# Performance work log

Measured on AMD Instinct MI355X. Metric: run time of the kernel, lower is better.

The kernel has to match this reference:

```python
import jax, jax.numpy as jnp
import numpy as np

N_NODES = 50000
N_EDGES = 800000
N_GRAPHS = 64
IN_C = 64
HID = 64
NEG_SLOPE = 0.2  # PyG GATConv default


def setup_inputs() -> dict:
    key = jax.random.key(0)
    ks = jax.random.split(key, 12)
    x = jax.random.normal(ks[0], (N_NODES, IN_C), dtype=jnp.float32)
    edge_index = jax.random.randint(ks[1], (2, N_EDGES), 0, N_NODES, dtype=jnp.int64)
    batch = jnp.sort(jax.random.randint(ks[2], (N_NODES,), 0, N_GRAPHS, dtype=jnp.int64))
    s = 1.0 / np.sqrt(IN_C)
    sh = 1.0 / np.sqrt(HID)
    W = jax.random.uniform(ks[3], (IN_C, HID), jnp.float32, -s, s)
    att_src = jax.random.uniform(ks[4], (HID,), jnp.float32, -sh, sh)
    att_dst = jax.random.uniform(ks[5], (HID,), jnp.float32, -sh, sh)
    bias_gat = jnp.zeros((HID,), jnp.float32)
    w1 = jax.random.uniform(ks[6], (HID, HID), jnp.float32, -sh, sh)
    b1 = jax.random.uniform(ks[7], (HID,), jnp.float32, -sh, sh)
    w2 = jax.random.uniform(ks[8], (HID, 1), jnp.float32, -sh, sh)
    b2 = jax.random.uniform(ks[9], (1,), jnp.float32, -sh, sh)
    return {"x": x, "edge_index": edge_index, "batch": batch, "W": W,
            "att_src": att_src, "att_dst": att_dst, "bias_gat": bias_gat,
            "w1": w1, "b1": b1, "w2": w2, "b2": b2}


def _gat_conv(x, edge_index, W, att_src, att_dst, bias_gat):
    N = x.shape[0]
    # add self-loops (PyG default)
    loops = jnp.arange(N, dtype=edge_index.dtype)
    src = jnp.concatenate([edge_index[0], loops])  # message source j
    dst = jnp.concatenate([edge_index[1], loops])  # message target i
    h = x @ W                                      # [N, HID]
    a_s = h @ att_src                              # [N]
    a_d = h @ att_dst                              # [N]
    e = jax.nn.leaky_relu(a_s[src] + a_d[dst], negative_slope=NEG_SLOPE)  # [E+N]
    # segment softmax over incoming edges of each target node
    m = jax.ops.segment_max(e, dst, num_segments=N)
    ex = jnp.exp(e - m[dst])
    denom = jax.ops.segment_sum(ex, dst, num_segments=N)
    alpha = ex / denom[dst]
    out = jax.ops.segment_sum(h[src] * alpha[:, None], dst, num_segments=N)
    return out + bias_gat


def reference(x, edge_index, batch, W, att_src, att_dst, bias_gat, w1, b1, w2, b2):
    h = jax.nn.relu(_gat_conv(x, edge_index, W, att_src, att_dst, bias_gat))
    # global mean pool over each graph
    sums = jax.ops.segment_sum(h, batch, num_segments=N_GRAPHS)          # [G, HID]
    cnt = jax.ops.segment_sum(jnp.ones((h.shape[0],), h.dtype), batch,
                              num_segments=N_GRAPHS)
    pooled = sums / jnp.maximum(cnt, 1.0)[:, None]
    z = jax.nn.relu(pooled @ w1 + b1)
    z = z @ w2 + b2
    return jax.nn.sigmoid(z)  # [G, 1]
```

## Files before the change

kernel.cpp:

```cpp
#include <hip/hip_runtime.h>

#define NN 50000
#define NE 800000
#define NG 64
#define HID 64
#define NEG 0.2f
#define NPW 64
#define NBUCK 196
#define CHUNK 2048
#define KC_CAP 6144

__global__ __launch_bounds__(256)
void k_xw(const float* __restrict__ x, const float* __restrict__ W,
          const float* __restrict__ att_s, const float* __restrict__ att_d,
          float* __restrict__ h, float* __restrict__ as_, float* __restrict__ ad_,
          int* __restrict__ gcur) {
    __shared__ __align__(16) float sW[64][64];
    __shared__ __align__(16) float sxT[64][68];
    int t = threadIdx.x;
    if (blockIdx.x == 0 && t < NBUCK) gcur[t] = 0;
    int r0 = blockIdx.x * 64;
    for (int i = t; i < 4096; i += 256) sW[i >> 6][i & 63] = W[i];
    for (int i = t; i < 4096; i += 256) {
        int r = i >> 6, c = i & 63;
        int gr = r0 + r; if (gr >= NN) gr = NN - 1;
        sxT[c][r] = x[(size_t)gr * 64 + c];
    }
    __syncthreads();

    int tx = t & 15, ty = t >> 4;
    float4 asv = ((const float4*)att_s)[tx];
    float4 adv = ((const float4*)att_d)[tx];

    float acc[4][4] = {};
    #pragma unroll
    for (int k = 0; k < 64; ++k) {
        float4 a = *(const float4*)&sxT[k][4 * ty];
        float4 b = *(const float4*)&sW[k][4 * tx];
        float av[4] = {a.x, a.y, a.z, a.w};
        float bv[4] = {b.x, b.y, b.z, b.w};
        #pragma unroll
        for (int i = 0; i < 4; ++i)
            #pragma unroll
            for (int j = 0; j < 4; ++j)
                acc[i][j] += av[i] * bv[j];
    }

    #pragma unroll
    for (int i = 0; i < 4; ++i) {
        int r = r0 + 4 * ty + i;
        if (r < NN) {
            float4 hv = make_float4(acc[i][0], acc[i][1], acc[i][2], acc[i][3]);
            *(float4*)&h[(size_t)r * 64 + 4 * tx] = hv;
            float ps = acc[i][0]*asv.x + acc[i][1]*asv.y + acc[i][2]*asv.z + acc[i][3]*asv.w;
            float pd = acc[i][0]*adv.x + acc[i][1]*adv.y + acc[i][2]*adv.z + acc[i][3]*adv.w;
            #pragma unroll
            for (int m = 1; m <= 8; m <<= 1) {
                ps += __shfl_xor(ps, m, 64);
                pd += __shfl_xor(pd, m, 64);
            }
            if (tx == 0) { as_[r] = ps; ad_[r] = pd; }
        }
    }
}

__global__ __launch_bounds__(256)
void k_bucket(const int* __restrict__ src, const int* __restrict__ dst,
              int* __restrict__ gcur, int* __restrict__ ebuf) {
    __shared__ int lhist[256], lscan[256], loff[256], lcur[256], gbase[256];
    __shared__ int lsort[CHUNK];
    __shared__ unsigned char lbuck[CHUNK];
    int t = threadIdx.x;
    int base = blockIdx.x * CHUNK;
    int cnt = NE - base; if (cnt > CHUNK) cnt = CHUNK; if (cnt < 0) cnt = 0;

    int ds[8], ss[8];
    int nv = 0;
    #pragma unroll
    for (int j = 0; j < 8; ++j) {
        int e = base + j * 256 + t;
        if (e < NE) { ds[nv] = dst[e]; ss[nv] = src[e]; ++nv; }
    }
    lhist[t] = 0;
    __syncthreads();
    for (int j = 0; j < nv; ++j) atomicAdd(&lhist[ds[j] >> 8], 1);
    __syncthreads();
    lscan[t] = lhist[t];
    __syncthreads();
    for (int off = 1; off < 256; off <<= 1) {
        int u = (t >= off) ? lscan[t - off] : 0;
        __syncthreads();
        lscan[t] += u;
        __syncthreads();
    }
    loff[t] = lscan[t] - lhist[t];
    lcur[t] = 0;
    __syncthreads();
    for (int j = 0; j < nv; ++j) {
        int b = ds[j] >> 8;
        int r = atomicAdd(&lcur[b], 1);
        int slot = loff[b] + r;
        lsort[slot] = (ss[j] << 8) | (ds[j] & 255);
        lbuck[slot] = (unsigned char)b;
    }
    if (t < NBUCK) {
        int c = lhist[t];
        gbase[t] = c ? atomicAdd(&gcur[t], c) : 0;
    }
    __syncthreads();
    for (int i = t; i < cnt; i += 256) {
        int b = lbuck[i];
        ebuf[b * KC_CAP + gbase[b] + (i - loff[b])] = lsort[i];
    }
}

__global__ __launch_bounds__(256)
void k_csr(const int* __restrict__ gcur, const int* __restrict__ ebuf,
           int* __restrict__ csr, int* __restrict__ cursor, int* __restrict__ deg) {
    __shared__ int lhist[256], lscan[256], loff[256], lcur[256], bscan[256];
    __shared__ int lsrc[KC_CAP];
    int t = threadIdx.x;
    int b = blockIdx.x;

    bscan[t] = (t < NBUCK) ? gcur[t] : 0;
    __syncthreads();
    for (int off = 1; off < 256; off <<= 1) {
        int u = (t >= off) ? bscan[t - off] : 0;
        __syncthreads();
        bscan[t] += u;
        __syncthreads();
    }
    int sz = gcur[b];
    int gb = bscan[b] - sz;
    const int* seg = ebuf + b * KC_CAP;

    lhist[t] = 0;
    __syncthreads();
    for (int i = t; i < sz; i += 256)
        atomicAdd(&lhist[seg[i] & 255], 1);
    __syncthreads();
    lscan[t] = lhist[t];
    __syncthreads();
    for (int off = 1; off < 256; off <<= 1) {
        int u = (t >= off) ? lscan[t - off] : 0;
        __syncthreads();
        lscan[t] += u;
        __syncthreads();
    }
    loff[t] = lscan[t] - lhist[t];
    lcur[t] = 0;
    __syncthreads();
    for (int i = t; i < sz; i += 256) {
        int w = seg[i];
        int dl = w & 255;
        int r = atomicAdd(&lcur[dl], 1);
        lsrc[loff[dl] + r] = w >> 8;
    }
    __syncthreads();
    for (int i = t; i < sz; i += 256)
        csr[gb + i] = lsrc[i];
    int d = b * 256 + t;
    if (d < NN) {
        deg[d] = lhist[t];
        cursor[d] = gb + loff[t] + lhist[t];
    }
}

__global__ __launch_bounds__(256)
void k_gather(const int* __restrict__ csr, const int* __restrict__ cursor,
              const int* __restrict__ deg, const float* __restrict__ h,
              const float* __restrict__ as_, const float* __restrict__ ad_,
              const float* __restrict__ bias, float* __restrict__ g,
              float* __restrict__ poolz) {
    int t = threadIdx.x;
    if (blockIdx.x == 0) {
        for (int i = t; i < NG * HID + NG; i += 256) poolz[i] = 0.f;
    }
    int wave = t >> 6, lane = t & 63;
    int d = blockIdx.x * 4 + wave;
    if (d >= NN) return;
    int cend = cursor[d];
    int nd   = deg[d];
    int cbeg = cend - nd;
    float adv = ad_[d];
    float e0 = as_[d] + adv;
    e0 = e0 >= 0.f ? e0 : NEG * e0;
    float ex0 = __expf(e0);
    float den = ex0;
    float acc = h[(size_t)d * 64 + lane] * ex0;
    #pragma unroll 4
    for (int c = cbeg; c < cend; ++c) {
        int s = csr[c];
        float av = as_[s] + adv;
        av = av >= 0.f ? av : NEG * av;
        float ex = __expf(av);
        den += ex;
        acc += h[(size_t)s * 64 + lane] * ex;
    }
    g[(size_t)d * 64 + lane] = fmaxf(acc / den + bias[lane], 0.f);
}

__global__ __launch_bounds__(256)
void k_node(const float* __restrict__ g, const int* __restrict__ batch,
            float* __restrict__ pooled, float* __restrict__ cnt) {
    int t = threadIdx.x;
    int wave = t >> 6, lane = t & 63;
    int n0 = (blockIdx.x * 4 + wave) * NPW;
    if (n0 >= NN) return;
    int n1 = n0 + NPW; if (n1 > NN) n1 = NN;
    float acc = 0.f, c = 0.f;
    int cur = batch[n0];
    for (int n = n0; n < n1; ++n) {
        int gr = batch[n];
        if (gr != cur) {
            atomicAdd(&pooled[cur * 64 + lane], acc);
            if (lane == 0) atomicAdd(&cnt[cur], c);
            acc = 0.f; c = 0.f; cur = gr;
        }
        acc += g[(size_t)n * 64 + lane];
        c += 1.f;
    }
    atomicAdd(&pooled[cur * 64 + lane], acc);
    if (lane == 0) atomicAdd(&cnt[cur], c);
}

__global__ __launch_bounds__(256)
void k_final(const float* __restrict__ pooled, const float* __restrict__ cnt,
             const float* __restrict__ w1, const float* __restrict__ b1,
             const float* __restrict__ w2, const float* __restrict__ b2,
             float* __restrict__ out) {
    __shared__ float sp[64][65];
    __shared__ float sz[64][65];
    int t = threadIdx.x;
    for (int i = t; i < 4096; i += 256) {
        int g = i >> 6, c = i & 63;
        sp[g][c] = pooled[i] / fmaxf(cnt[g], 1.0f);
    }
    __syncthreads();
    for (int i = t; i < 4096; i += 256) {
        int g = i >> 6, c = i & 63;
        float acc = b1[c];
        #pragma unroll
        for (int k = 0; k < 64; ++k) acc += sp[g][k] * w1[k * 64 + c];
        sz[g][c] = fmaxf(acc, 0.f);
    }
    __syncthreads();
    if (t < 64) {
        float acc = b2[0];
        #pragma unroll
        for (int c = 0; c < 64; ++c) acc += sz[t][c] * w2[c];
        out[t] = 1.f / (1.f + __expf(-acc));
    }
}

extern "C" void kernel_launch(void* const* d_in, const int* in_sizes, int n_in,
                              void* d_out, int out_size, void* d_ws, size_t ws_size,
                              hipStream_t stream) {
    const float* x     = (const float*)d_in[0];
    const int*   ei    = (const int*)d_in[1];
    const int*   batch = (const int*)d_in[2];
    const float* W     = (const float*)d_in[3];
    const float* att_s = (const float*)d_in[4];
    const float* att_d = (const float*)d_in[5];
    const float* bias  = (const float*)d_in[6];
    const float* w1    = (const float*)d_in[7];
    const float* b1    = (const float*)d_in[8];
    const float* w2    = (const float*)d_in[9];
    const float* b2    = (const float*)d_in[10];
    float* out = (float*)d_out;

    const int* src = ei;
    const int* dst = ei + NE;

    float* h      = (float*)d_ws;
    float* as_    = h + (size_t)NN * HID;
    float* ad_    = as_ + NN;
    float* g      = ad_ + NN;
    float* pooled = g + (size_t)NN * HID;
    float* cntp   = pooled + NG * HID;
    int*   deg    = (int*)(cntp + NG);
    int*   cursor = deg + NN;
    int*   csr    = cursor + NN;
    int*   gcur   = csr + NE;
    int*   ebuf   = (int*)g;


    k_xw<<<(NN + 63) / 64, 256, 0, stream>>>(x, W, att_s, att_d, h, as_, ad_, gcur);

    k_bucket<<<(NE + CHUNK - 1) / CHUNK, 256, 0, stream>>>(src, dst, gcur, ebuf);
    k_csr<<<NBUCK, 256, 0, stream>>>(gcur, ebuf, csr, cursor, deg);

    k_gather<<<(NN + 3) / 4, 256, 0, stream>>>(csr, cursor, deg, h, as_, ad_, bias, g, pooled);

    k_node<<<(NN / (4 * NPW)) + 1, 256, 0, stream>>>(g, batch, pooled, cntp);

    k_final<<<1, 256, 0, stream>>>(pooled, cntp, w1, b1, w2, b2, out);
}
```

Before: 143.8 us.

## Fuse CSR build, gather and pooling into one bucketed LDS-accumulate kernel with bf16 features

Drops the separate CSR sort, per-node gather and pooling kernels. Each block now owns a 128-node bucket and accumulates exp-weighted messages into shared memory with LDS atomics, then applies the normalization, ReLU and pooling directly. The edge exp weights are computed during bucketing and stored alongside the packed src/dst, and h is stored as bf16 to halve gather bandwidth. This removes the intermediate CSR and g buffers and several launches. The cost is only 392 blocks of parallelism, heavy LDS atomic contention, and reduced precision of h, which may affect tolerance.

```diff
diff --git a/kernel.cpp b/kernel.cpp
--- a/kernel.cpp
+++ b/kernel.cpp
@@ -1,24 +1,37 @@
 #include <hip/hip_runtime.h>
+#include <hip/hip_bf16.h>
 
 #define NN 50000
 #define NE 800000
 #define NG 64
 #define HID 64
 #define NEG 0.2f
-#define NPW 64
-#define NBUCK 196
+#define NBUCK 392
 #define CHUNK 2048
-#define KC_CAP 6144
+#define KC_CAP 3072
+#define ROWP 66
+
+__device__ __forceinline__ unsigned short f2bf(float f) {
+    unsigned int u = __float_as_uint(f);
+    unsigned int r = (u + 0x7FFF + ((u >> 16) & 1)) >> 16;
+    return (unsigned short)r;
+}
+__device__ __forceinline__ float bf_lo(unsigned int p) { return __uint_as_float(p << 16); }
+__device__ __forceinline__ float bf_hi(unsigned int p) { return __uint_as_float(p & 0xFFFF0000u); }
+__device__ __forceinline__ float bf2f(unsigned short b) { return __uint_as_float(((unsigned int)b) << 16); }
 
 __global__ __launch_bounds__(256)
 void k_xw(const float* __restrict__ x, const float* __restrict__ W,
           const float* __restrict__ att_s, const float* __restrict__ att_d,
-          float* __restrict__ h, float* __restrict__ as_, float* __restrict__ ad_,
-          int* __restrict__ gcur) {
+          unsigned short* __restrict__ hb, float* __restrict__ as_, float* __restrict__ ad_,
+          int* __restrict__ gcur, float* __restrict__ poolz) {
     __shared__ __align__(16) float sW[64][64];
     __shared__ __align__(16) float sxT[64][68];
     int t = threadIdx.x;
-    if (blockIdx.x == 0 && t < NBUCK) gcur[t] = 0;
+    if (blockIdx.x == 0) {
+        for (int i = t; i < NBUCK; i += 256) gcur[i] = 0;
+        for (int i = t; i < NG * HID + NG; i += 256) poolz[i] = 0.f;
+    }
     int r0 = blockIdx.x * 64;
     for (int i = t; i < 4096; i += 256) sW[i >> 6][i & 63] = W[i];
     for (int i = t; i < 4096; i += 256) {
@@ -50,8 +63,10 @@
     for (int i = 0; i < 4; ++i) {
         int r = r0 + 4 * ty + i;
         if (r < NN) {
-            float4 hv = make_float4(acc[i][0], acc[i][1], acc[i][2], acc[i][3]);
-            *(float4*)&h[(size_t)r * 64 + 4 * tx] = hv;
+            ushort4 hv;
+            hv.x = f2bf(acc[i][0]); hv.y = f2bf(acc[i][1]);
+            hv.z = f2bf(acc[i][2]); hv.w = f2bf(acc[i][3]);
+            *(ushort4*)&hb[(size_t)r * 64 + 4 * tx] = hv;
             float ps = acc[i][0]*asv.x + acc[i][1]*asv.y + acc[i][2]*asv.z + acc[i][3]*asv.w;
             float pd = acc[i][0]*adv.x + acc[i][1]*adv.y + acc[i][2]*adv.z + acc[i][3]*adv.w;
             #pragma unroll
@@ -64,30 +79,37 @@
     }
 }
 
-__global__ __launch_bounds__(256)
+__global__ __launch_bounds__(512)
 void k_bucket(const int* __restrict__ src, const int* __restrict__ dst,
-              int* __restrict__ gcur, int* __restrict__ ebuf) {
-    __shared__ int lhist[256], lscan[256], loff[256], lcur[256], gbase[256];
-    __shared__ int lsort[CHUNK];
-    __shared__ unsigned char lbuck[CHUNK];
+              const float* __restrict__ as_, const float* __restrict__ ad_,
+              int* __restrict__ gcur, int2* __restrict__ ebuf) {
+    __shared__ int lhist[512], lscan[512], loff[512], lcur[512], gbase[512];
+    __shared__ int2 lsort[CHUNK];
+    __shared__ unsigned short lbuck[CHUNK];
     int t = threadIdx.x;
     int base = blockIdx.x * CHUNK;
     int cnt = NE - base; if (cnt > CHUNK) cnt = CHUNK; if (cnt < 0) cnt = 0;
 
-    int ds[8], ss[8];
+    int ds[4], ss[4];
+    float ex[4];
     int nv = 0;
     #pragma unroll
-    for (int j = 0; j < 8; ++j) {
-        int e = base + j * 256 + t;
+    for (int j = 0; j < 4; ++j) {
+        int e = base + j * 512 + t;
         if (e < NE) { ds[nv] = dst[e]; ss[nv] = src[e]; ++nv; }
     }
+    for (int j = 0; j < nv; ++j) {
+        float e = as_[ss[j]] + ad_[ds[j]];
+        e = e >= 0.f ? e : NEG * e;
+        ex[j] = __expf(e);
+    }
     lhist[t] = 0;
     __syncthreads();
-    for (int j = 0; j < nv; ++j) atomicAdd(&lhist[ds[j] >> 8], 1);
+    for (int j = 0; j < nv; ++j) atomicAdd(&lhist[ds[j] >> 7], 1);
     __syncthreads();
     lscan[t] = lhist[t];
     __syncthreads();
-    for (int off = 1; off < 256; off <<= 1) {
+    for (int off = 1; off < 512; off <<= 1) {
         int u = (t >= off) ? lscan[t - off] : 0;
         __syncthreads();
         lscan[t] += u;
@@ -97,131 +119,94 @@
     lcur[t] = 0;
     __syncthreads();
     for (int j = 0; j < nv; ++j) {
-        int b = ds[j] >> 8;
+        int b = ds[j] >> 7;
         int r = atomicAdd(&lcur[b], 1);
         int slot = loff[b] + r;
-        lsort[slot] = (ss[j] << 8) | (ds[j] & 255);
-        lbuck[slot] = (unsigned char)b;
+        lsort[slot] = make_int2((ss[j] << 7) | (ds[j] & 127), __float_as_int(ex[j]));
+        lbuck[slot] = (unsigned short)b;
     }
     if (t < NBUCK) {
         int c = lhist[t];
         gbase[t] = c ? atomicAdd(&gcur[t], c) : 0;
     }
     __syncthreads();
-    for (int i = t; i < cnt; i += 256) {
+    for (int i = t; i < cnt; i += 512) {
         int b = lbuck[i];
         ebuf[b * KC_CAP + gbase[b] + (i - loff[b])] = lsort[i];
     }
 }
 
 __global__ __launch_bounds__(256)
-void k_csr(const int* __restrict__ gcur, const int* __restrict__ ebuf,
-           int* __restrict__ csr, int* __restrict__ cursor, int* __restrict__ deg) {
-    __shared__ int lhist[256], lscan[256], loff[256], lcur[256], bscan[256];
-    __shared__ int lsrc[KC_CAP];
-    int t = threadIdx.x;
+void k_merged(const int* __restrict__ gcur, const int2* __restrict__ ebuf,
+              const unsigned short* __restrict__ hb,
+              const float* __restrict__ as_, const float* __restrict__ ad_,
+              const float* __restrict__ bias, const int* __restrict__ batch,
+              float* __restrict__ pooled, float* __restrict__ cnt) {
+    __shared__ float lacc[128 * ROWP];
+    __shared__ float lden[128];
+    int t = threadIdx.x;
+    int wave = t >> 6, lane = t & 63;
+    int grp = lane >> 3, cc = lane & 7;
     int b = blockIdx.x;
 
-    bscan[t] = (t < NBUCK) ? gcur[t] : 0;
-    __syncthreads();
-    for (int off = 1; off < 256; off <<= 1) {
-        int u = (t >= off) ? bscan[t - off] : 0;
-        __syncthreads();
-        bscan[t] += u;
-        __syncthreads();
-    }
+    for (int i = t; i < 128 * ROWP; i += 256) lacc[i] = 0.f;
+    if (t < 128) lden[t] = 0.f;
+    __syncthreads();
+
     int sz = gcur[b];
-    int gb = bscan[b] - sz;
-    const int* seg = ebuf + b * KC_CAP;
-
-    lhist[t] = 0;
-    __syncthreads();
-    for (int i = t; i < sz; i += 256)
-        atomicAdd(&lhist[seg[i] & 255], 1);
-    __syncthreads();
-    lscan[t] = lhist[t];
-    __syncthreads();
-    for (int off = 1; off < 256; off <<= 1) {
-        int u = (t >= off) ? lscan[t - off] : 0;
-        __syncthreads();
-        lscan[t] += u;
-        __syncthreads();
-    }
-    loff[t] = lscan[t] - lhist[t];
-    lcur[t] = 0;
-    __syncthreads();
-    for (int i = t; i < sz; i += 256) {
-        int w = seg[i];
-        int dl = w & 255;
-        int r = atomicAdd(&lcur[dl], 1);
-        lsrc[loff[dl] + r] = w >> 8;
-    }
-    __syncthreads();
-    for (int i = t; i < sz; i += 256)
-        csr[gb + i] = lsrc[i];
-    int d = b * 256 + t;
-    if (d < NN) {
-        deg[d] = lhist[t];
-        cursor[d] = gb + loff[t] + lhist[t];
-    }
-}
-
-__global__ __launch_bounds__(256)
-void k_gather(const int* __restrict__ csr, const int* __restrict__ cursor,
-              const int* __restrict__ deg, const float* __restrict__ h,
-              const float* __restrict__ as_, const float* __restrict__ ad_,
-              const float* __restrict__ bias, float* __restrict__ g,
-              float* __restrict__ poolz) {
-    int t = threadIdx.x;
-    if (blockIdx.x == 0) {
-        for (int i = t; i < NG * HID + NG; i += 256) poolz[i] = 0.f;
-    }
-    int wave = t >> 6, lane = t & 63;
-    int d = blockIdx.x * 4 + wave;
-    if (d >= NN) return;
-    int cend = cursor[d];
-    int nd   = deg[d];
-    int cbeg = cend - nd;
-    float adv = ad_[d];
-    float e0 = as_[d] + adv;
-    e0 = e0 >= 0.f ? e0 : NEG * e0;
-    float ex0 = __expf(e0);
-    float den = ex0;
-    float acc = h[(size_t)d * 64 + lane] * ex0;
-    #pragma unroll 4
-    for (int c = cbeg; c < cend; ++c) {
-        int s = csr[c];
-        float av = as_[s] + adv;
-        av = av >= 0.f ? av : NEG * av;
-        float ex = __expf(av);
-        den += ex;
-        acc += h[(size_t)s * 64 + lane] * ex;
-    }
-    g[(size_t)d * 64 + lane] = fmaxf(acc / den + bias[lane], 0.f);
-}
-
-__global__ __launch_bounds__(256)
-void k_node(const float* __restrict__ g, const int* __restrict__ batch,
-            float* __restrict__ pooled, float* __restrict__ cnt) {
-    int t = threadIdx.x;
-    int wave = t >> 6, lane = t & 63;
-    int n0 = (blockIdx.x * 4 + wave) * NPW;
-    if (n0 >= NN) return;
-    int n1 = n0 + NPW; if (n1 > NN) n1 = NN;
-    float acc = 0.f, c = 0.f;
-    int cur = batch[n0];
-    for (int n = n0; n < n1; ++n) {
-        int gr = batch[n];
+    const int2* seg = ebuf + b * KC_CAP;
+
+    for (int i0 = wave * 8; i0 < sz; i0 += 32) {
+        int e = i0 + grp;
+        if (e < sz) {
+            int2 w = seg[e];
+            int   s  = w.x >> 7;
+            int   dl = w.x & 127;
+            float ex = __int_as_float(w.y);
+            uint4 v = *(const uint4*)&hb[(size_t)s * 64 + 8 * cc];
+            float* a = &lacc[dl * ROWP + 8 * cc];
+            atomicAdd(a + 0, bf_lo(v.x) * ex);
+            atomicAdd(a + 1, bf_hi(v.x) * ex);
+            atomicAdd(a + 2, bf_lo(v.y) * ex);
+            atomicAdd(a + 3, bf_hi(v.y) * ex);
+            atomicAdd(a + 4, bf_lo(v.z) * ex);
+            atomicAdd(a + 5, bf_hi(v.z) * ex);
+            atomicAdd(a + 6, bf_lo(v.w) * ex);
+            atomicAdd(a + 7, bf_hi(v.w) * ex);
+            if (cc == 0) atomicAdd(&lden[dl], ex);
+        }
+    }
+    __syncthreads();
+
+    float bl = bias[lane];
+    int dbase = b * 128 + wave * 32;
+    float racc = 0.f, rcnt = 0.f;
+    int cur = -1;
+    for (int k = 0; k < 32; ++k) {
+        int d = dbase + k;
+        if (d >= NN) break;
+        int gr = batch[d];
         if (gr != cur) {
-            atomicAdd(&pooled[cur * 64 + lane], acc);
-            if (lane == 0) atomicAdd(&cnt[cur], c);
-            acc = 0.f; c = 0.f; cur = gr;
+            if (cur >= 0) {
+                atomicAdd(&pooled[cur * 64 + lane], racc);
+                if (lane == 0) atomicAdd(&cnt[cur], rcnt);
+            }
+            racc = 0.f; rcnt = 0.f; cur = gr;
         }
-        acc += g[(size_t)n * 64 + lane];
-        c += 1.f;
-    }
-    atomicAdd(&pooled[cur * 64 + lane], acc);
-    if (lane == 0) atomicAdd(&cnt[cur], c);
+        float e0 = as_[d] + ad_[d];
+        e0 = e0 >= 0.f ? e0 : NEG * e0;
+        float ex0 = __expf(e0);
+        int r = wave * 32 + k;
+        float hs = bf2f(hb[(size_t)d * 64 + lane]);
+        float num = lacc[r * ROWP + lane] + ex0 * hs;
+        float den = lden[r] + ex0;
+        float val = fmaxf(num / den + bl, 0.f);
+        racc += val; rcnt += 1.f;
+    }
+    if (cur >= 0) {
+        atomicAdd(&pooled[cur * 64 + lane], racc);
+        if (lane == 0) atomicAdd(&cnt[cur], rcnt);
+    }
 }
 
 __global__ __launch_bounds__(256)
@@ -272,27 +257,19 @@
     const int* src = ei;
     const int* dst = ei + NE;
 
-    float* h      = (float*)d_ws;
-    float* as_    = h + (size_t)NN * HID;
+    unsigned short* hb = (unsigned short*)d_ws;
+    float* as_    = (float*)(hb + (size_t)NN * HID);
     float* ad_    = as_ + NN;
-    float* g      = ad_ + NN;
-    float* pooled = g + (size_t)NN * HID;
+    float* pooled = ad_ + NN;
     float* cntp   = pooled + NG * HID;
-    int*   deg    = (int*)(cntp + NG);
-    int*   cursor = deg + NN;
-    int*   csr    = cursor + NN;
-    int*   gcur   = csr + NE;
-    int*   ebuf   = (int*)g;
-
-
-    k_xw<<<(NN + 63) / 64, 256, 0, stream>>>(x, W, att_s, att_d, h, as_, ad_, gcur);
-
-    k_bucket<<<(NE + CHUNK - 1) / CHUNK, 256, 0, stream>>>(src, dst, gcur, ebuf);
-    k_csr<<<NBUCK, 256, 0, stream>>>(gcur, ebuf, csr, cursor, deg);
-
-    k_gather<<<(NN + 3) / 4, 256, 0, stream>>>(csr, cursor, deg, h, as_, ad_, bias, g, pooled);
-
-    k_node<<<(NN / (4 * NPW)) + 1, 256, 0, stream>>>(g, batch, pooled, cntp);
+    int*   gcur   = (int*)(cntp + NG);
+    int2*  ebuf   = (int2*)(gcur + NBUCK);
+
+    k_xw<<<(NN + 63) / 64, 256, 0, stream>>>(x, W, att_s, att_d, hb, as_, ad_, gcur, pooled);
+
+    k_bucket<<<(NE + CHUNK - 1) / CHUNK, 512, 0, stream>>>(src, dst, as_, ad_, gcur, ebuf);
+
+    k_merged<<<NBUCK, 256, 0, stream>>>(gcur, ebuf, hb, as_, ad_, bias, batch, pooled, cntp);
 
     k_final<<<1, 256, 0, stream>>>(pooled, cntp, w1, b1, w2, b2, out);
 }
```

After: 441.8 us. 3.07x slower.
